# Optimization experiments

Measured on AMD Instinct MI355X. Metric: run time of the kernel, lower is better.

The kernel has to match this reference:

```python
import jax, jax.numpy as jnp
import numpy as np

NUM_REL = 20000
NUM_EDGES = 640000
DIM_IN = 128
DIM_OUT = 128
NUM_HEAD = 8
DIM_HID = DIM_OUT // NUM_HEAD
NUM_BIN = 10
NEG_SLOPE = 0.2


def leaky_relu(x):
    return jnp.where(x >= 0, x, NEG_SLOPE * x)


def setup_inputs() -> dict:
    key = jax.random.key(0)
    ks = jax.random.split(key, 8)
    emb_rel = jax.random.normal(ks[0], (NUM_REL, DIM_IN), dtype=jnp.float32)
    head = jax.random.randint(ks[1], (NUM_EDGES, 1), 0, NUM_REL)
    tail = jax.random.randint(ks[2], (NUM_EDGES, 1), 0, NUM_REL)
    bins = jax.random.randint(ks[3], (NUM_EDGES, 1), 0, NUM_BIN)
    relation_triplets = jnp.concatenate([head, tail, bins], axis=-1).astype(jnp.int64)
    # xavier-normal-ish init
    attn_proj_w = jax.random.normal(ks[4], (DIM_OUT, 2 * DIM_IN), dtype=jnp.float32) * (2.0 / np.sqrt(2 * DIM_IN + DIM_OUT))
    attn_proj_b = jnp.zeros((DIM_OUT,), dtype=jnp.float32)
    attn_bin = jax.random.normal(ks[5], (NUM_BIN, NUM_HEAD, 1), dtype=jnp.float32) * 0.3
    attn_vec = jax.random.normal(ks[6], (1, NUM_HEAD, DIM_HID), dtype=jnp.float32) * (2.0 / np.sqrt(NUM_HEAD * DIM_HID))
    aggr_proj_w = jax.random.normal(ks[7], (DIM_OUT, DIM_IN), dtype=jnp.float32) * (2.0 / np.sqrt(DIM_IN + DIM_OUT))
    aggr_proj_b = jnp.zeros((DIM_OUT,), dtype=jnp.float32)
    return {"emb_rel": emb_rel, "relation_triplets": relation_triplets,
            "attn_proj_w": attn_proj_w, "attn_proj_b": attn_proj_b,
            "attn_bin": attn_bin, "attn_vec": attn_vec,
            "aggr_proj_w": aggr_proj_w, "aggr_proj_b": aggr_proj_b}


def reference(emb_rel, relation_triplets, attn_proj_w, attn_proj_b, attn_bin, attn_vec, aggr_proj_w, aggr_proj_b):
    num_rel = emb_rel.shape[0]
    head = relation_triplets[..., 0]
    tail = relation_triplets[..., 1]
    bins = relation_triplets[..., 2]
    # edge gather + concat: [E, 2*dim_in]
    concat = jnp.concatenate([emb_rel[head], emb_rel[tail]], axis=-1)
    proj = concat @ attn_proj_w.T + attn_proj_b  # [E, dim_out]
    proj = leaky_relu(proj).reshape(-1, NUM_HEAD, DIM_HID)
    attn_raw = (proj * attn_vec).sum(axis=-1, keepdims=True) + leaky_relu(attn_bin[bins])  # [E,H,1]
    # per-head-relation segment softmax over edges grouped by head index
    seg_max = jax.ops.segment_max(attn_raw, head, num_segments=num_rel)  # [R,H,1]
    attn_val = jnp.exp(attn_raw - seg_max[head])
    seg_sum = jax.ops.segment_sum(attn_val, head, num_segments=num_rel)  # [R,H,1]
    beta = attn_val / (seg_sum[head] + 1e-16)
    msg = (emb_rel[tail] @ aggr_proj_w.T + aggr_proj_b).reshape(-1, NUM_HEAD, DIM_HID)
    out = jax.ops.segment_sum(beta * msg, head, num_segments=num_rel)  # [R,H,Dh]
    return out.reshape(num_rel, -1)
```

## Files before the change

kernel.cpp:

```cpp
#include <hip/hip_runtime.h>
#include <hip/hip_bf16.h>
#include <cstdint>
#include <cstddef>

#define NUM_REL    20000
#define NUM_EDGES  640000
#define DIM        128
#define NUM_HEAD   8
#define DIM_HID    16
#define NUM_BIN    10
#define CAP        128
#define CNT_STR    16
#define PROJ_BLKS  471
#define SCAT_BLKS  625
#define PREP_BLKS  1250

using u16 = unsigned short;
using u32 = unsigned int;
typedef __attribute__((ext_vector_type(8))) short bf16x8;
typedef __attribute__((ext_vector_type(4))) float f32x4;

__device__ __forceinline__ float b2f(u16 u) { return __uint_as_float(((u32)u) << 16); }
__device__ __forceinline__ float lo2f(u32 u) { return __uint_as_float(u << 16); }
__device__ __forceinline__ float hi2f(u32 u) { return __uint_as_float(u & 0xffff0000u); }
__device__ __forceinline__ float lrelu(float x) { return fmaxf(x, 0.2f * x); }
__device__ __forceinline__ int clampi(int v, int hi) { return v < 0 ? 0 : (v > hi ? hi : v); }
__device__ __forceinline__ float ldf(const void* p, int f32m, int i)
{ return f32m ? ((const float*)p)[i] : b2f(((const u16*)p)[i]); }
__device__ __forceinline__ u16 f2b(float x)
{ u32 u = __float_as_uint(x); u += 0x7fffu + ((u >> 16) & 1u); return (u16)(u >> 16); }
__device__ __forceinline__ u32 pk2(float a, float b)
{ return (u32)f2b(a) | ((u32)f2b(b) << 16); }

__device__ __forceinline__ void detect_flags(const int* __restrict__ trip,
                                             const u16* __restrict__ emb,
                                             int* sF, int tid)
{
    if (tid < 64) {
        bool odd_zero = (trip[2 * tid + 1] == 0) && (trip[2 * tid + 129] == 0);
        unsigned long long m1 = __ballot(odd_zero);
        int ex = (emb[2 * tid] >> 7) & 0xFF;
        bool inr = (ex >= 110) && (ex <= 136);
        unsigned long long m2 = __ballot(inr);
        if (tid == 0) {
            sF[0] = (~m1 == 0ull) ? 1 : 0;
            sF[1] = (__popcll(m2) >= 32) ? 0 : 1;
        }
    }
    __syncthreads();
}

__global__ __launch_bounds__(256) void k_prep(
    const void* __restrict__ emb, const int* __restrict__ trip,
    u16* __restrict__ Eb, int* __restrict__ cnt)
{
    __shared__ int sF[2];
    const int tid = threadIdx.x;
    detect_flags(trip, (const u16*)emb, sF, tid);
    const int f32m = sF[1];

    const int g = blockIdx.x * 256 + tid;
    cnt[g] = 0;
    if (f32m) {
        const float4* src = (const float4*)emb;
        float4 x0 = src[2 * g], x1 = src[2 * g + 1];
        uint4 o;
        o.x = pk2(x0.x, x0.y); o.y = pk2(x0.z, x0.w);
        o.z = pk2(x1.x, x1.y); o.w = pk2(x1.z, x1.w);
        ((uint4*)Eb)[g] = o;
    } else {
        ((uint4*)Eb)[g] = ((const uint4*)emb)[g];
    }
}

__global__ __launch_bounds__(256) void k_projscatter(
    const u16* __restrict__ Eb, const int* __restrict__ trip,
    const void* __restrict__ emb,
    const void* __restrict__ w_attn, const void* __restrict__ w_aggr,
    const void* __restrict__ b_attn, const void* __restrict__ b_aggr,
    float* __restrict__ A, u16* __restrict__ BM,
    int* __restrict__ cnt, int* __restrict__ bucket)
{
    __shared__ u16 sW[128 * 64];
    __shared__ float sBias[128];
    __shared__ int sF[2];

    const int tid = threadIdx.x;
    detect_flags(trip, (const u16*)emb, sF, tid);
    const int is64 = sF[0], f32m = sF[1];

    if (blockIdx.x >= PROJ_BLKS) {
        const int e0 = ((blockIdx.x - PROJ_BLKS) * 256 + tid) * 4;
        int h[4], t[4], b[4], p[4];
        if (is64) {
            const int4* w = (const int4*)(trip + 6 * e0);
            int4 w0 = w[0], w1 = w[1], w2 = w[2], w3 = w[3], w4 = w[4], w5 = w[5];
            h[0] = w0.x; t[0] = w0.z; b[0] = w1.x;
            h[1] = w1.z; t[1] = w2.x; b[1] = w2.z;
            h[2] = w3.x; t[2] = w3.z; b[2] = w4.x;
            h[3] = w4.z; t[3] = w5.x; b[3] = w5.z;
        } else {
            const int4* w = (const int4*)(trip + 3 * e0);
            int4 w0 = w[0], w1 = w[1], w2 = w[2];
            h[0] = w0.x; t[0] = w0.y; b[0] = w0.z;
            h[1] = w0.w; t[1] = w1.x; b[1] = w1.y;
            h[2] = w1.z; t[2] = w1.w; b[2] = w2.x;
            h[3] = w2.y; t[3] = w2.z; b[3] = w2.w;
        }
        #pragma unroll
        for (int i = 0; i < 4; ++i) {
            h[i] = clampi(h[i], NUM_REL - 1);
            t[i] = clampi(t[i], NUM_REL - 1);
            b[i] = clampi(b[i], NUM_BIN - 1);
        }
        #pragma unroll
        for (int i = 0; i < 4; ++i) p[i] = atomicAdd(&cnt[h[i] * CNT_STR], 1);
        #pragma unroll
        for (int i = 0; i < 4; ++i)
            if (p[i] < CAP) bucket[h[i] * CAP + p[i]] = t[i] | (b[i] << 20);
        return;
    }

    const int mt = blockIdx.x / 3, nt = blockIdx.x % 3;
    const int r0 = mt * 128;

    if (tid < 128)
        sBias[tid] = (nt == 0) ? 0.f : ldf((nt == 1) ? b_attn : b_aggr, f32m, tid);

    const void* wsrc = (nt == 2) ? w_aggr : w_attn;
    const int stride = (nt == 2) ? 128 : 256;
    const int koff   = (nt == 1) ? 128 : 0;

    const int lane = tid & 63, wid = tid >> 6;
    const int wm = (wid >> 1) * 64, wn = (wid & 1) * 64;
    const int ln15 = lane & 15, q = lane >> 4;

    int arow[4];
    #pragma unroll
    for (int mi = 0; mi < 4; ++mi) {
        int g = r0 + wm + mi * 16 + ln15;
        arow[mi] = (g < NUM_REL) ? g : (NUM_REL - 1);
    }

    f32x4 acc[4][4] = {};
    #pragma unroll
    for (int kh = 0; kh < 2; ++kh) {
        if (kh) __syncthreads();
        if (f32m) {
            const float* src = (const float*)wsrc;
            #pragma unroll
            for (int i = 0; i < 8; ++i) {
                int f = i * 256 + tid;
                int row = f >> 4, pos = f & 15;
                const float* rp = src + (size_t)row * stride + koff + kh * 64;
                float4 x = ((const float4*)rp)[pos];
                int chunk = (pos >> 1) ^ (row & 7);
                *(uint2*)&sW[row * 64 + chunk * 8 + (pos & 1) * 4] =
                    make_uint2(pk2(x.x, x.y), pk2(x.z, x.w));
            }
        } else {
            const u16* src = (const u16*)wsrc;
            #pragma unroll
            for (int i = 0; i < 4; ++i) {
                int f = i * 256 + tid;
                int row = f >> 3, pos = f & 7;
                const u16* rp = src + (size_t)row * stride + koff + kh * 64;
                uint4 x = ((const uint4*)rp)[pos];
                int chunk = pos ^ (row & 7);
                *(uint4*)&sW[row * 64 + chunk * 8] = x;
            }
        }
        __syncthreads();

        #pragma unroll
        for (int k2 = 0; k2 < 2; ++k2) {
            const int kkg = kh * 2 + k2;
            const int kc = (kkg * 4 + q) * 8;
            const int cl = (k2 * 4 + q) ^ (ln15 & 7);
            bf16x8 a[4], b[4];
            #pragma unroll
            for (int mi = 0; mi < 4; ++mi)
                a[mi] = *(const bf16x8*)(Eb + (size_t)arow[mi] * DIM + kc);
            #pragma unroll
            for (int ni = 0; ni < 4; ++ni) {
                int n = wn + ni * 16 + ln15;
                b[ni] = *(const bf16x8*)&sW[n * 64 + cl * 8];
            }
            #pragma unroll
            for (int mi = 0; mi < 4; ++mi)
                #pragma unroll
                for (int ni = 0; ni < 4; ++ni)
                    acc[mi][ni] = __builtin_amdgcn_mfma_f32_16x16x32_bf16(
                        a[mi], b[ni], acc[mi][ni], 0, 0, 0);
        }
    }

    #pragma unroll
    for (int mi = 0; mi < 4; ++mi) {
        #pragma unroll
        for (int reg = 0; reg < 4; ++reg) {
            int g = r0 + wm + mi * 16 + q * 4 + reg;
            if (g < NUM_REL) {
                #pragma unroll
                for (int ni = 0; ni < 4; ++ni) {
                    int c = wn + ni * 16 + ln15;
                    float v = acc[mi][ni][reg] + sBias[c];
                    if (nt == 0) {
                        A[(size_t)g * DIM + c] = v;
                    } else {
                        size_t o = (size_t)g * 256 + (size_t)((c >> 4) * 32)
                                 + (c & 15) + (nt == 2 ? 16 : 0);
                        BM[o] = f2b(v);
                    }
                }
            }
        }
    }
}

__global__ __launch_bounds__(256, 4) void k_segment(
    const float* __restrict__ A, const u16* __restrict__ BM,
    const void* __restrict__ attn_bin, const void* __restrict__ attn_vec,
    const int* __restrict__ cnt, const int* __restrict__ bucket,
    const int* __restrict__ trip, const void* __restrict__ emb,
    void* __restrict__ out)
{
    __shared__ float sAr[4][DIM];
    __shared__ float sVec[DIM];
    __shared__ float sBin[NUM_BIN * NUM_HEAD];
    __shared__ int sF[2];

    const int tid  = threadIdx.x;
    detect_flags(trip, (const u16*)emb, sF, tid);
    const int f32m = sF[1];

    const int wid  = tid >> 6, lane = tid & 63;
    const int r = blockIdx.x * 4 + wid;
    int nE = cnt[r * CNT_STR]; if (nE > CAP) nE = CAP;
    const int* __restrict__ bk = bucket + r * CAP;

    {
        const float2* ap = (const float2*)(A + (size_t)r * DIM);
        float2 a2 = ap[lane];
        sAr[wid][2 * lane] = a2.x; sAr[wid][2 * lane + 1] = a2.y;
    }
    if (tid < DIM) sVec[tid] = ldf(attn_vec, f32m, tid);
    else if (tid < DIM + NUM_BIN * NUM_HEAD)
        sBin[tid - DIM] = lrelu(ldf(attn_bin, f32m, tid - DIM));
    __syncthreads();

    if (nE == 0) {
        if (f32m) ((float2*)out)[(size_t)r * 64 + lane] = make_float2(0.f, 0.f);
        else      ((u32*)out)[(size_t)r * 64 + lane] = 0;
        return;
    }

    const int el = lane >> 3, hd = lane & 7;

    float av[16], vv[16];
    {
        const float4* pA = (const float4*)(&sAr[wid][hd * DIM_HID]);
        const float4* pV = (const float4*)(&sVec[hd * DIM_HID]);
        #pragma unroll
        for (int i = 0; i < 4; ++i) {
            float4 a4 = pA[i], v4 = pV[i];
            av[4*i+0]=a4.x; av[4*i+1]=a4.y; av[4*i+2]=a4.z; av[4*i+3]=a4.w;
            vv[4*i+0]=v4.x; vv[4*i+1]=v4.y; vv[4*i+2]=v4.z; vv[4*i+3]=v4.w;
        }
    }

    const u16* __restrict__ BMh = BM + hd * 32;

    int tba = (el      < nE) ? bk[el]     : 0;
    int tbb = (8 + el  < nE) ? bk[8 + el] : 0;
    int ia = tba & 0xFFFFF, ib = tbb & 0xFFFFF;
    uint4 qa0, qa1, qb0, qb1;
    {
        const uint4* Ba = (const uint4*)(BMh + (size_t)ia * 256);
        const uint4* Bc = (const uint4*)(BMh + (size_t)ib * 256);
        qa0 = Ba[0]; qa1 = Ba[1];
        qb0 = Bc[0]; qb1 = Bc[1];
    }

    float l = 0.f;
    float acc[16];
    #pragma unroll
    for (int j = 0; j < 16; ++j) acc[j] = 0.f;

    for (int base = 0; base < nE; base += 16) {
        uint4 ma0, ma1, mb0, mb1;
        {
            const uint4* Ma = (const uint4*)(BMh + (size_t)ia * 256 + 16);
            const uint4* Mc = (const uint4*)(BMh + (size_t)ib * 256 + 16);
            ma0 = Ma[0]; ma1 = Ma[1];
            mb0 = Mc[0]; mb1 = Mc[1];
        }
        const int bsa = (tba >> 20) & 0xF;
        const int bsb = (tbb >> 20) & 0xF;

        int ea_n  = base + 16 + el;
        int eb_n  = base + 24 + el;
        int tba_n = (ea_n < nE) ? bk[ea_n] : 0;
        int tbb_n = (eb_n < nE) ? bk[eb_n] : 0;
        int ia_n  = tba_n & 0xFFFFF, ib_n = tbb_n & 0xFFFFF;
        uint4 qa0n, qa1n, qb0n, qb1n;
        {
            const uint4* Ban = (const uint4*)(BMh + (size_t)ia_n * 256);
            const uint4* Bcn = (const uint4*)(BMh + (size_t)ib_n * 256);
            qa0n = Ban[0]; qa1n = Ban[1];
            qb0n = Bcn[0]; qb1n = Bcn[1];
        }

        float sa0 = sBin[bsa * NUM_HEAD + hd];
        float sb0 = sBin[bsb * NUM_HEAD + hd];
        sa0 = fmaf(lrelu(av[0]  + lo2f(qa0.x)), vv[0],  sa0);
        sb0 = fmaf(lrelu(av[0]  + lo2f(qb0.x)), vv[0],  sb0);
        float sa1 = lrelu(av[1] + hi2f(qa0.x)) * vv[1];
        float sb1 = lrelu(av[1] + hi2f(qb0.x)) * vv[1];
        float sa2 = lrelu(av[2] + lo2f(qa0.y)) * vv[2];
        float sb2 = lrelu(av[2] + lo2f(qb0.y)) * vv[2];
        float sa3 = lrelu(av[3] + hi2f(qa0.y)) * vv[3];
        float sb3 = lrelu(av[3] + hi2f(qb0.y)) * vv[3];
        sa0 = fmaf(lrelu(av[4]  + lo2f(qa0.z)), vv[4],  sa0);
        sb0 = fmaf(lrelu(av[4]  + lo2f(qb0.z)), vv[4],  sb0);
        sa1 = fmaf(lrelu(av[5]  + hi2f(qa0.z)), vv[5],  sa1);
        sb1 = fmaf(lrelu(av[5]  + hi2f(qb0.z)), vv[5],  sb1);
        sa2 = fmaf(lrelu(av[6]  + lo2f(qa0.w)), vv[6],  sa2);
        sb2 = fmaf(lrelu(av[6]  + lo2f(qb0.w)), vv[6],  sb2);
        sa3 = fmaf(lrelu(av[7]  + hi2f(qa0.w)), vv[7],  sa3);
        sb3 = fmaf(lrelu(av[7]  + hi2f(qb0.w)), vv[7],  sb3);
        sa0 = fmaf(lrelu(av[8]  + lo2f(qa1.x)), vv[8],  sa0);
        sb0 = fmaf(lrelu(av[8]  + lo2f(qb1.x)), vv[8],  sb0);
        sa1 = fmaf(lrelu(av[9]  + hi2f(qa1.x)), vv[9],  sa1);
        sb1 = fmaf(lrelu(av[9]  + hi2f(qb1.x)), vv[9],  sb1);
        sa2 = fmaf(lrelu(av[10] + lo2f(qa1.y)), vv[10], sa2);
        sb2 = fmaf(lrelu(av[10] + lo2f(qb1.y)), vv[10], sb2);
        sa3 = fmaf(lrelu(av[11] + hi2f(qa1.y)), vv[11], sa3);
        sb3 = fmaf(lrelu(av[11] + hi2f(qb1.y)), vv[11], sb3);
        sa0 = fmaf(lrelu(av[12] + lo2f(qa1.z)), vv[12], sa0);
        sb0 = fmaf(lrelu(av[12] + lo2f(qb1.z)), vv[12], sb0);
        sa1 = fmaf(lrelu(av[13] + hi2f(qa1.z)), vv[13], sa1);
        sb1 = fmaf(lrelu(av[13] + hi2f(qb1.z)), vv[13], sb1);
        sa2 = fmaf(lrelu(av[14] + lo2f(qa1.w)), vv[14], sa2);
        sb2 = fmaf(lrelu(av[14] + lo2f(qb1.w)), vv[14], sb2);
        sa3 = fmaf(lrelu(av[15] + hi2f(qa1.w)), vv[15], sa3);
        sb3 = fmaf(lrelu(av[15] + hi2f(qb1.w)), vv[15], sb3);
        float sa = (sa0 + sa1) + (sa2 + sa3);
        float sb = (sb0 + sb1) + (sb2 + sb3);
        sa = fminf(fmaxf(sa, -60.f), 60.f);
        sb = fminf(fmaxf(sb, -60.f), 60.f);
        float pa = ((base + el)     < nE) ? __expf(sa) : 0.f;
        float pb = ((base + 8 + el) < nE) ? __expf(sb) : 0.f;
        l += pa + pb;

        {
            const u32* wa = (const u32*)&ma0;
            const u32* wb = (const u32*)&mb0;
            #pragma unroll
            for (int j = 0; j < 4; ++j) {
                acc[2*j]   = fmaf(pa, lo2f(wa[j]), acc[2*j]);
                acc[2*j+1] = fmaf(pa, hi2f(wa[j]), acc[2*j+1]);
                acc[2*j]   = fmaf(pb, lo2f(wb[j]), acc[2*j]);
                acc[2*j+1] = fmaf(pb, hi2f(wb[j]), acc[2*j+1]);
            }
            const u32* xa = (const u32*)&ma1;
            const u32* xb = (const u32*)&mb1;
            #pragma unroll
            for (int j = 0; j < 4; ++j) {
                acc[8+2*j]   = fmaf(pa, lo2f(xa[j]), acc[8+2*j]);
                acc[8+2*j+1] = fmaf(pa, hi2f(xa[j]), acc[8+2*j+1]);
                acc[8+2*j]   = fmaf(pb, lo2f(xb[j]), acc[8+2*j]);
                acc[8+2*j+1] = fmaf(pb, hi2f(xb[j]), acc[8+2*j+1]);
            }
        }

        tba = tba_n; tbb = tbb_n; ia = ia_n; ib = ib_n;
        qa0 = qa0n; qa1 = qa1n; qb0 = qb0n; qb1 = qb1n;
    }

    float lt = l + __shfl_xor(l, 8);
    lt += __shfl_xor(lt, 16);
    lt += __shfl_xor(lt, 32);
    float inv = 1.0f / (lt + 1e-16f);

    #pragma unroll
    for (int j = 0; j < 16; ++j) {
        float v = acc[j];
        v += __shfl_xor(v, 8);
        v += __shfl_xor(v, 16);
        v += __shfl_xor(v, 32);
        acc[j] = v * inv;
    }

    if (el == 0) {
        if (f32m) {
            float* op = (float*)out + (size_t)r * DIM + hd * DIM_HID;
            #pragma unroll
            for (int j = 0; j < 4; ++j) {
                float4 v4 = make_float4(acc[4*j], acc[4*j+1], acc[4*j+2], acc[4*j+3]);
                ((float4*)op)[j] = v4;
            }
        } else {
            u32* op = (u32*)out + (size_t)r * 64 + hd * 8;
            #pragma unroll
            for (int j = 0; j < 8; ++j)
                op[j] = pk2(acc[2*j], acc[2*j+1]);
        }
    }
}

extern "C" void kernel_launch(void* const* d_in, const int* in_sizes, int n_in,
                              void* d_out, int out_size, void* d_ws, size_t ws_size,
                              hipStream_t stream)
{
    (void)in_sizes; (void)n_in; (void)out_size; (void)ws_size;
    const void* emb      = d_in[0];
    const int*  trip     = (const int*)d_in[1];
    const void* w_attn   = d_in[2];
    const void* b_attn   = d_in[3];
    const void* attn_bin = d_in[4];
    const void* attn_vec = d_in[5];
    const void* w_aggr   = d_in[6];
    const void* b_aggr   = d_in[7];

    char* p = (char*)d_ws;
    float* A      = (float*)p; p += (size_t)NUM_REL * DIM * 4;
    u16*   BM     = (u16*)p;   p += (size_t)NUM_REL * 256 * 2;
    int*   bucket = (int*)p;   p += (size_t)NUM_REL * CAP * 4;
    int*   cnt    = (int*)p;   p += (size_t)NUM_REL * CNT_STR * 4;
    u16*   Eb     = (u16*)p;   p += (size_t)NUM_REL * DIM * 2;

    k_prep<<<PREP_BLKS, 256, 0, stream>>>(emb, trip, Eb, cnt);
    k_projscatter<<<PROJ_BLKS + SCAT_BLKS, 256, 0, stream>>>(
        Eb, trip, emb, w_attn, w_aggr, b_attn, b_aggr, A, BM, cnt, bucket);
    k_segment<<<NUM_REL / 4, 256, 0, stream>>>(A, BM, attn_bin, attn_vec,
                                               cnt, bucket, trip, emb, d_out);
}
```

Before: 164.9 us.

## Partition per-relation edge buckets by block to reduce atomic contention

The edge scatter now spreads each head relation's counter and bucket across 8 partitions chosen by block index, so atomics from different blocks hit different counter slots in the padded cnt row. The segment kernel sums the 8 partition counts into prefix offsets and compacts the partitioned bucket entries into shared memory before the existing softmax and aggregation loop. This is meant to reduce atomic serialization on hot counters. In exchange the bucket workspace doubles, the segment kernel gains an extra gather pass and shared-memory footprint, and the per-partition cap of 32 could drop edges if a partition overflows.

```diff
diff --git a/kernel.cpp b/kernel.cpp
--- a/kernel.cpp
+++ b/kernel.cpp
@@ -9,7 +9,8 @@
 #define NUM_HEAD   8
 #define DIM_HID    16
 #define NUM_BIN    10
-#define CAP        128
+#define NPART      8
+#define CAP_P      32
 #define CNT_STR    16
 #define PROJ_BLKS  471
 #define SCAT_BLKS  625
@@ -90,6 +91,7 @@
     const int is64 = sF[0], f32m = sF[1];
 
     if (blockIdx.x >= PROJ_BLKS) {
+        const int part = blockIdx.x & (NPART - 1);
         const int e0 = ((blockIdx.x - PROJ_BLKS) * 256 + tid) * 4;
         int h[4], t[4], b[4], p[4];
         if (is64) {
@@ -114,10 +116,13 @@
             b[i] = clampi(b[i], NUM_BIN - 1);
         }
         #pragma unroll
-        for (int i = 0; i < 4; ++i) p[i] = atomicAdd(&cnt[h[i] * CNT_STR], 1);
-        #pragma unroll
         for (int i = 0; i < 4; ++i)
-            if (p[i] < CAP) bucket[h[i] * CAP + p[i]] = t[i] | (b[i] << 20);
+            p[i] = atomicAdd(&cnt[h[i] * CNT_STR + part], 1);
+        #pragma unroll
+        for (int i = 0; i < 4; ++i)
+            if (p[i] < CAP_P)
+                bucket[h[i] * (NPART * CAP_P) + part * CAP_P + p[i]] =
+                    t[i] | (b[i] << 20);
         return;
     }
 
@@ -228,6 +233,7 @@
     __shared__ float sAr[4][DIM];
     __shared__ float sVec[DIM];
     __shared__ float sBin[NUM_BIN * NUM_HEAD];
+    __shared__ int sBK[4][NPART * CAP_P];
     __shared__ int sF[2];
 
     const int tid  = threadIdx.x;
@@ -236,8 +242,20 @@
 
     const int wid  = tid >> 6, lane = tid & 63;
     const int r = blockIdx.x * 4 + wid;
-    int nE = cnt[r * CNT_STR]; if (nE > CAP) nE = CAP;
-    const int* __restrict__ bk = bucket + r * CAP;
+
+    int Pp[8], nE;
+    {
+        const int4* c4 = (const int4*)(cnt + (size_t)r * CNT_STR);
+        int4 ca = c4[0], cb = c4[1];
+        int cc[8] = { ca.x, ca.y, ca.z, ca.w, cb.x, cb.y, cb.z, cb.w };
+        int run = 0;
+        #pragma unroll
+        for (int p = 0; p < 8; ++p) {
+            int c = cc[p]; c = c < CAP_P ? c : CAP_P;
+            Pp[p] = run; run += c;
+        }
+        nE = run;
+    }
 
     {
         const float2* ap = (const float2*)(A + (size_t)r * DIM);
@@ -254,6 +272,17 @@
         else      ((u32*)out)[(size_t)r * 64 + lane] = 0;
         return;
     }
+
+    {
+        const int* bkg = bucket + (size_t)r * (NPART * CAP_P);
+        for (int e = lane; e < nE; e += 64) {
+            int p = 0;
+            #pragma unroll
+            for (int qq = 1; qq < 8; ++qq) p += (e >= Pp[qq]) ? 1 : 0;
+            sBK[wid][e] = bkg[p * CAP_P + (e - Pp[p])];
+        }
+    }
+    const int* __restrict__ bk = sBK[wid];
 
     const int el = lane >> 3, hd = lane & 7;
 
@@ -426,7 +455,7 @@
     char* p = (char*)d_ws;
     float* A      = (float*)p; p += (size_t)NUM_REL * DIM * 4;
     u16*   BM     = (u16*)p;   p += (size_t)NUM_REL * 256 * 2;
-    int*   bucket = (int*)p;   p += (size_t)NUM_REL * CAP * 4;
+    int*   bucket = (int*)p;   p += (size_t)NUM_REL * NPART * CAP_P * 4;
     int*   cnt    = (int*)p;   p += (size_t)NUM_REL * CNT_STR * 4;
     u16*   Eb     = (u16*)p;   p += (size_t)NUM_REL * DIM * 2;
 
```

After: 169.5 us. +2.8%, slower.
